# Optimization experiments

Measured on AMD Instinct MI355X. Metric: run time of the kernel, lower is better.

The kernel has to match this reference:

```python
import jax, jax.numpy as jnp
import numpy as np

T, B, H = 2048, 8, 16
KF, VF, KS, VS = 32, 64, 128, 64


def _l2norm(x, eps=1e-6):
    return x / jnp.sqrt(jnp.sum(x * x, axis=-1, keepdims=True) + eps)


def setup_inputs() -> dict:
    key = jax.random.key(0)
    ks = jax.random.split(key, 12)
    # k/q are L2-normalized externally (per E88/E90 kernel contract)
    k_fast = _l2norm(jax.random.normal(ks[0], (T, B, H, KF), jnp.float32))
    q_fast = _l2norm(jax.random.normal(ks[1], (T, B, H, KF), jnp.float32))
    v_fast = jax.random.normal(ks[2], (T, B, H, VF), jnp.float32)
    k_slow = _l2norm(jax.random.normal(ks[3], (T, B, H, KS), jnp.float32))
    q_slow = _l2norm(jax.random.normal(ks[4], (T, B, H, KS), jnp.float32))
    v_slow = jax.random.normal(ks[5], (T, B, H, VS), jnp.float32)
    # decay factors in (0.85, 1.0): typical Mamba2-style per-head scalar decay
    decay_fast = 0.85 + 0.15 * jax.random.uniform(ks[6], (T, B, H), jnp.float32)
    decay_slow = 0.85 + 0.15 * jax.random.uniform(ks[7], (T, B, H), jnp.float32)
    slow_gate = jax.random.uniform(ks[8], (T, B, H), jnp.float32)
    mix_fast = jax.random.uniform(ks[9], (T, B, H), jnp.float32)
    mix_slow = jax.random.uniform(ks[10], (T, B, H), jnp.float32)
    S_fast0 = jnp.zeros((B, H, KF, VF), jnp.float32)
    S_slow0 = jnp.zeros((B, H, KS, VS), jnp.float32)
    return dict(k_fast=k_fast, v_fast=v_fast, q_fast=q_fast, decay_fast=decay_fast,
                k_slow=k_slow, v_slow=v_slow, q_slow=q_slow, decay_slow=decay_slow,
                slow_gate=slow_gate, mix_fast=mix_fast, mix_slow=mix_slow,
                S_fast0=S_fast0, S_slow0=S_slow0, n_heads=H)


def _e90_scan(k_fast, v_fast, q_fast, decay_fast,
              k_slow, v_slow, q_slow, decay_slow,
              slow_gate, mix_fast, mix_slow, S_fast0, S_slow0):
    def step(carry, x):
        S_f, S_s = carry  # [B,H,KF,VF], [B,H,KS,VS]
        kf, vf, qf, df, ksl, vsl, qsl, dsl, g, mf, ms = x
        # fast state: updated every timestep (decay + rank-1 outer product)
        S_f = df[..., None, None] * S_f + kf[..., :, None] * vf[..., None, :]
        # slow state: gated soft update
        S_s_new = dsl[..., None, None] * S_s + ksl[..., :, None] * vsl[..., None, :]
        g_ = g[..., None, None]
        S_s = g_ * S_s_new + (1.0 - g_) * S_s
        out_f = jnp.einsum('bhk,bhkv->bhv', qf, S_f)
        out_s = jnp.einsum('bhk,bhkv->bhv', qsl, S_s)
        out = mf[..., None] * out_f + ms[..., None] * out_s
        return (S_f, S_s), out

    xs = (k_fast, v_fast, q_fast, decay_fast,
          k_slow, v_slow, q_slow, decay_slow,
          slow_gate, mix_fast, mix_slow)
    (S_f_final, S_s_final), output = jax.lax.scan(step, (S_fast0, S_slow0), xs)
    return S_f_final, S_s_final, output  # output: [T,B,H,VF]


def reference(k_fast, v_fast, q_fast, decay_fast, k_slow, v_slow, q_slow,
              decay_slow, slow_gate, mix_fast, mix_slow, S_fast0, S_slow0, n_heads):
    return _e90_scan(k_fast, v_fast, q_fast, decay_fast,
                     k_slow, v_slow, q_slow, decay_slow,
                     slow_gate, mix_fast, mix_slow, S_fast0, S_slow0)
```

## Files before the change

kernel.cpp:

```cpp
#include <hip/hip_runtime.h>

#define T_STEPS 2048
#define BH      128
#define KS_     128
#define VS_     64
#define KF_     32
#define VF_     64
#define LCH     32
#define NCG     32
#define NC      (T_STEPS / LCH)
#define HALF_T  1024
#define NTHR    512
#define NTHRA   256
#define WSLOT   5120
#define SCLS_OFF 1310720
#define SCLF_OFF 1835008
#define RUN_OFF  2359296
#define WS_NEEDED_BYTES ((size_t)(RUN_OFF + 512) * 4)
#define SOFF    (BH*KF_*VF_)
#define YOFF    (BH*KF_*VF_ + BH*KS_*VS_)

typedef __attribute__((ext_vector_type(8))) short short8;
typedef __attribute__((ext_vector_type(16))) float f32x16;

#define MFMA32(a,b,c) __builtin_amdgcn_mfma_f32_32x32x16_bf16((a),(b),(c),0,0,0)
#define CROW(r,hi) (((r)&3) + 8*((r)>>2) + 4*(hi))

__device__ __forceinline__ unsigned short f2b(float x) {
    union { float f; unsigned u; } v; v.f = x;
    unsigned r = v.u + 0x7FFFu + ((v.u >> 16) & 1u);
    return (unsigned short)(r >> 16);
}
__device__ __forceinline__ unsigned cvtpk(float lo, float hi_) {
    unsigned r;
    asm("v_cvt_pk_bf16_f32 %0, %1, %2" : "=v"(r) : "v"(lo), "v"(hi_));
    return r;
}
__device__ __forceinline__ short8 ld8(const unsigned short* p) {
    return *(const short8*)p;
}

__global__ __launch_bounds__(NTHRA, 2)
void e90_scan(const float* __restrict__ k_fast,  const float* __restrict__ v_fast,
              const float* __restrict__ q_fast,  const float* __restrict__ decay_fast,
              const float* __restrict__ k_slow,  const float* __restrict__ v_slow,
              const float* __restrict__ q_slow,  const float* __restrict__ decay_slow,
              const float* __restrict__ slow_gate, const float* __restrict__ mix_fast,
              const float* __restrict__ mix_slow, const float* __restrict__ S_fast0,
              const float* __restrict__ S_slow0, float* __restrict__ dout,
              float* __restrict__ dws)
{
    __shared__ __align__(16) unsigned short Qs [LCH][136];
    __shared__ __align__(16) unsigned short Ksl[LCH][136];
    __shared__ __align__(16) unsigned short Sbs[LCH][136];
    __shared__ __align__(16) unsigned short Psl[LCH][40];
    __shared__ __align__(16) unsigned short Pfl[LCH][40];
    __shared__ __align__(16) unsigned short Qfl[LCH][40];
    __shared__ __align__(16) unsigned short Kfl[LCH][40];
    __shared__ __align__(16) unsigned short Sbfl[LCH][40];
    __shared__ __align__(16) unsigned short VTs[2][LCH][40];
    __shared__ __align__(16) unsigned short VTf[2][LCH][40];

    const int tid  = threadIdx.x;
    const int bid  = blockIdx.x;
    const int xcd  = bid & 7;
    const int q8   = bid >> 3;
    const int p    = xcd * 16 + (q8 >> 2);
    const int vh   = (q8 >> 1) & 1;
    const int v0   = vh * 32;
    const int th   = q8 & 1;
    const int tgb  = th * HALF_T;
    const int slot = p * 2 + vh;
    const int lane = tid & 63;
    const int wid  = tid >> 6;
    const int l31  = lane & 31;
    const int hi   = lane >> 5;
    const int s_   = tid >> 3;
    const int sub  = tid & 7;
    const int k0_  = sub * 16;
    const int j0_  = sub * 4;

    float* out_y = dout + YOFF;

    f32x16 St0, St1, oacc;
#pragma unroll
    for (int r = 0; r < 16; ++r) { St0[r] = 0.0f; St1[r] = 0.0f; oacc[r] = 0.0f; }
    if (th == 0) {
        if (wid < 2) {
#pragma unroll
            for (int r = 0; r < 16; ++r) {
                St0[r] = S_slow0[((size_t)p*KS_ + 32*(2*wid)   + CROW(r,hi))*VS_ + v0 + l31];
                St1[r] = S_slow0[((size_t)p*KS_ + 32*(2*wid+1) + CROW(r,hi))*VS_ + v0 + l31];
            }
        } else if (wid == 2) {
#pragma unroll
            for (int r = 0; r < 16; ++r)
                St0[r] = S_fast0[((size_t)p*KF_ + CROW(r,hi))*VF_ + v0 + l31];
        }
    }
    if (wid < 2) {
#pragma unroll
        for (int r = 0; r < 16; ++r) {
            Sbs[l31][32*(2*wid)   + CROW(r,hi)] = f2b(St0[r]);
            Sbs[l31][32*(2*wid+1) + CROW(r,hi)] = f2b(St1[r]);
        }
    } else if (wid == 2) {
#pragma unroll
        for (int r = 0; r < 16; ++r) Sbfl[l31][CROW(r,hi)] = f2b(St0[r]);
    }

    float4 pK0,pK1,pK2,pK3, pQ0,pQ1,pQ2,pQ3, pVs,pVf,pKf,pQf;
    float pL0 = 0.f, pL1 = 0.f, pL2 = 0.f;

#define LOADCHUNK(CIDX) do {                                                    \
    int tc_ = (CIDX); if (tc_ > NCG-1) tc_ = NCG-1;                             \
    const int tb_ = tgb + tc_ * LCH;                                            \
    const float* bk_ = k_slow + ((size_t)(tb_+s_)*BH + p)*KS_ + k0_;            \
    pK0 = *(const float4*)bk_;      pK1 = *(const float4*)(bk_+4);              \
    pK2 = *(const float4*)(bk_+8);  pK3 = *(const float4*)(bk_+12);             \
    const float* bq_ = q_slow + ((size_t)(tb_+s_)*BH + p)*KS_ + k0_;            \
    pQ0 = *(const float4*)bq_;      pQ1 = *(const float4*)(bq_+4);              \
    pQ2 = *(const float4*)(bq_+8);  pQ3 = *(const float4*)(bq_+12);             \
    pVs = *(const float4*)(v_slow + ((size_t)(tb_+s_)*BH + p)*VS_ + v0 + j0_);  \
    pVf = *(const float4*)(v_fast + ((size_t)(tb_+s_)*BH + p)*VF_ + v0 + j0_);  \
    pKf = *(const float4*)(k_fast + ((size_t)(tb_+s_)*BH + p)*KF_ + j0_);       \
    pQf = *(const float4*)(q_fast + ((size_t)(tb_+s_)*BH + p)*KF_ + j0_);       \
    const size_t so_ = (size_t)(tb_ + l31)*BH + p;                              \
    pL0 = (hi ? decay_fast : decay_slow)[so_];                                  \
    pL1 = (hi ? mix_fast   : slow_gate )[so_];                                  \
    pL2 = hi ? 0.0f : mix_slow[so_];                                            \
    } while (0)

    LOADCHUNK(0);

    float bls = 1.f, blf = 1.f, ib = 1.f, ibf = 1.f, qsc = 0.f, qfc = 0.f, g_s = 0.f;
    float runAcc = 1.0f;

    for (int c = 0; c < NCG; ++c) {
        const int cb = c & 1;
        if (c > 0) {
            if (wid < 2) {
#pragma unroll
                for (int r = 0; r < 16; ++r) {
                    Sbs[l31][32*(2*wid)   + CROW(r,hi)] = f2b(St0[r]);
                    Sbs[l31][32*(2*wid+1) + CROW(r,hi)] = f2b(St1[r]);
                }
            } else if (wid == 2) {
#pragma unroll
                for (int r = 0; r < 16; ++r) Sbfl[l31][CROW(r,hi)] = f2b(St0[r]);
            } else {
                const int pb = cb ^ 1;
                f32x16 o2;
#pragma unroll
                for (int r = 0; r < 16; ++r) o2[r] = 0.0f;
                const unsigned short* ar = &Psl[l31][0];
                const unsigned short* br = &VTs[pb][l31][0];
                oacc = MFMA32(ld8(ar + 8*hi),      ld8(br + 8*hi),      oacc);
                oacc = MFMA32(ld8(ar + 16 + 8*hi), ld8(br + 16 + 8*hi), oacc);
                const unsigned short* af = &Pfl[l31][0];
                const unsigned short* bf = &VTf[pb][l31][0];
                o2 = MFMA32(ld8(af + 8*hi),      ld8(bf + 8*hi),      o2);
                o2 = MFMA32(ld8(af + 16 + 8*hi), ld8(bf + 16 + 8*hi), o2);
#pragma unroll
                for (int r = 0; r < 16; ++r) {
                    int tr = CROW(r,hi);
                    out_y[((size_t)(tgb + (c-1)*LCH + tr)*BH + p)*VF_ + v0 + l31] = oacc[r] + o2[r];
                }
            }
        }
        {
            float a = hi ? pL0 : __builtin_fmaf(pL1, pL0, 1.0f - pL1);
            float b = a;
#pragma unroll
            for (int d = 1; d < 32; d <<= 1) {
                float y = __shfl_up(b, d, 32);
                if (l31 >= d) b *= y;
            }
            if (th == 1 && wid == 0) {
                float sc = (hi ? pL1 : pL2) * b * runAcc;
                float* wsp = dws + (hi ? SCLF_OFF : SCLS_OFF) + (size_t)slot*HALF_T + c*LCH + l31;
                *wsp = sc;
            }
            float bs_s = __shfl(b, s_);
            float bf_s = __shfl(b, 32 + s_);
            bls = __shfl(b, 31);
            blf = __shfl(b, 63);
            g_s = __shfl(pL1, s_);
            float mf_s = __shfl(pL1, 32 + s_);
            float ms_s = __shfl(pL2, s_);
            ib  = 1.0f / bs_s;
            ibf = 1.0f / bf_s;
            qsc = ms_s * bs_s;
            qfc = mf_s * bf_s;
            runAcc *= (hi ? blf : bls);
        }
        {
            uint4 kw0, kw1, qw0, qw1;
            kw0.x = cvtpk(pK0.x*ib, pK0.y*ib);  kw0.y = cvtpk(pK0.z*ib, pK0.w*ib);
            kw0.z = cvtpk(pK1.x*ib, pK1.y*ib);  kw0.w = cvtpk(pK1.z*ib, pK1.w*ib);
            kw1.x = cvtpk(pK2.x*ib, pK2.y*ib);  kw1.y = cvtpk(pK2.z*ib, pK2.w*ib);
            kw1.z = cvtpk(pK3.x*ib, pK3.y*ib);  kw1.w = cvtpk(pK3.z*ib, pK3.w*ib);
            qw0.x = cvtpk(pQ0.x*qsc, pQ0.y*qsc); qw0.y = cvtpk(pQ0.z*qsc, pQ0.w*qsc);
            qw0.z = cvtpk(pQ1.x*qsc, pQ1.y*qsc); qw0.w = cvtpk(pQ1.z*qsc, pQ1.w*qsc);
            qw1.x = cvtpk(pQ2.x*qsc, pQ2.y*qsc); qw1.y = cvtpk(pQ2.z*qsc, pQ2.w*qsc);
            qw1.z = cvtpk(pQ3.x*qsc, pQ3.y*qsc); qw1.w = cvtpk(pQ3.z*qsc, pQ3.w*qsc);
            *(uint4*)&Ksl[s_][k0_]   = kw0;
            *(uint4*)&Ksl[s_][k0_+8] = kw1;
            *(uint4*)&Qs [s_][k0_]   = qw0;
            *(uint4*)&Qs [s_][k0_+8] = qw1;

            VTs[cb][j0_+0][s_] = f2b(g_s*pVs.x);
            VTs[cb][j0_+1][s_] = f2b(g_s*pVs.y);
            VTs[cb][j0_+2][s_] = f2b(g_s*pVs.z);
            VTs[cb][j0_+3][s_] = f2b(g_s*pVs.w);
            VTf[cb][j0_+0][s_] = f2b(pVf.x);
            VTf[cb][j0_+1][s_] = f2b(pVf.y);
            VTf[cb][j0_+2][s_] = f2b(pVf.z);
            VTf[cb][j0_+3][s_] = f2b(pVf.w);
            uint2 kf2; kf2.x = cvtpk(pKf.x*ibf, pKf.y*ibf); kf2.y = cvtpk(pKf.z*ibf, pKf.w*ibf);
            *(uint2*)&Kfl[s_][j0_] = kf2;
            uint2 qf2; qf2.x = cvtpk(pQf.x*qfc, pQf.y*qfc); qf2.y = cvtpk(pQf.z*qfc, pQf.w*qfc);
            *(uint2*)&Qfl[s_][j0_] = qf2;
        }
        __syncthreads();

        LOADCHUNK(c + 1);

        if (wid < 2) {
            const unsigned short* bv = &VTs[cb][l31][0];
            short8 b1 = ld8(bv + 8*hi);
            short8 b2 = ld8(bv + 16 + 8*hi);
            {
                const int T = 2*wid;
                short8 a1, a2;
#pragma unroll
                for (int e = 0; e < 8; ++e) {
                    a1[e] = (short)Ksl[8*hi + e][32*T + l31];
                    a2[e] = (short)Ksl[16 + 8*hi + e][32*T + l31];
                }
                St0 = MFMA32(a1, b1, St0);
                St0 = MFMA32(a2, b2, St0);
#pragma unroll
                for (int r = 0; r < 16; ++r) St0[r] *= bls;
            }
            {
                const int T = 2*wid + 1;
                short8 a1, a2;
#pragma unroll
                for (int e = 0; e < 8; ++e) {
                    a1[e] = (short)Ksl[8*hi + e][32*T + l31];
                    a2[e] = (short)Ksl[16 + 8*hi + e][32*T + l31];
                }
                St1 = MFMA32(a1, b1, St1);
                St1 = MFMA32(a2, b2, St1);
#pragma unroll
                for (int r = 0; r < 16; ++r) St1[r] *= bls;
            }
        } else if (wid == 2) {
            {
                short8 a1, a2;
#pragma unroll
                for (int e = 0; e < 8; ++e) {
                    a1[e] = (short)Kfl[8*hi + e][l31];
                    a2[e] = (short)Kfl[16 + 8*hi + e][l31];
                }
                const unsigned short* bv = &VTf[cb][l31][0];
                St0 = MFMA32(a1, ld8(bv + 8*hi),      St0);
                St0 = MFMA32(a2, ld8(bv + 16 + 8*hi), St0);
#pragma unroll
                for (int r = 0; r < 16; ++r) St0[r] *= blf;
            }
            {
                f32x16 p1;
#pragma unroll
                for (int r = 0; r < 16; ++r) p1[r] = 0.0f;
                const unsigned short* ar = &Qfl[l31][0];
                const unsigned short* br = &Kfl[l31][0];
                p1 = MFMA32(ld8(ar + 8*hi),      ld8(br + 8*hi),      p1);
                p1 = MFMA32(ld8(ar + 16 + 8*hi), ld8(br + 16 + 8*hi), p1);
#pragma unroll
                for (int r = 0; r < 16; ++r) {
                    int tr = CROW(r,hi);
                    Pfl[tr][l31] = f2b(tr >= l31 ? p1[r] : 0.0f);
                }
            }
            {
                f32x16 p1, p2;
#pragma unroll
                for (int r = 0; r < 16; ++r) { p1[r] = 0.0f; p2[r] = 0.0f; }
                const unsigned short* ar = &Qs [l31][0];
                const unsigned short* br = &Ksl[l31][0];
                const int kb = 8*hi;
#pragma unroll
                for (int st = 0; st < 8; st += 2) {
                    p1 = MFMA32(ld8(ar + kb + 16*st),     ld8(br + kb + 16*st),     p1);
                    p2 = MFMA32(ld8(ar + kb + 16*(st+1)), ld8(br + kb + 16*(st+1)), p2);
                }
#pragma unroll
                for (int r = 0; r < 16; ++r) {
                    int tr = CROW(r,hi);
                    Psl[tr][l31] = f2b(tr >= l31 ? p1[r] + p2[r] : 0.0f);
                }
            }
        } else {
            f32x16 o1, o2;
#pragma unroll
            for (int r = 0; r < 16; ++r) { o1[r] = 0.0f; o2[r] = 0.0f; }
            const unsigned short* ar = &Qs [l31][0];
            const unsigned short* br = &Sbs[l31][0];
            const int kb = 8*hi;
#pragma unroll
            for (int st = 0; st < 8; st += 2) {
                o1 = MFMA32(ld8(ar + kb + 16*st),     ld8(br + kb + 16*st),     o1);
                o2 = MFMA32(ld8(ar + kb + 16*(st+1)), ld8(br + kb + 16*(st+1)), o2);
            }
            const unsigned short* af = &Qfl [l31][0];
            const unsigned short* bf = &Sbfl[l31][0];
            o1 = MFMA32(ld8(af + 8*hi),      ld8(bf + 8*hi),      o1);
            o2 = MFMA32(ld8(af + 16 + 8*hi), ld8(bf + 16 + 8*hi), o2);
#pragma unroll
            for (int r = 0; r < 16; ++r) oacc[r] = o1[r] + o2[r];
        }
        __syncthreads();
    }

    if (wid == 3) {
        const int pb = (NCG - 1) & 1;
        f32x16 o2;
#pragma unroll
        for (int r = 0; r < 16; ++r) o2[r] = 0.0f;
        const unsigned short* ar = &Psl[l31][0];
        const unsigned short* br = &VTs[pb][l31][0];
        oacc = MFMA32(ld8(ar + 8*hi),      ld8(br + 8*hi),      oacc);
        oacc = MFMA32(ld8(ar + 16 + 8*hi), ld8(br + 16 + 8*hi), oacc);
        const unsigned short* af = &Pfl[l31][0];
        const unsigned short* bf = &VTf[pb][l31][0];
        o2 = MFMA32(ld8(af + 8*hi),      ld8(bf + 8*hi),      o2);
        o2 = MFMA32(ld8(af + 16 + 8*hi), ld8(bf + 16 + 8*hi), o2);
#pragma unroll
        for (int r = 0; r < 16; ++r) {
            int tr = CROW(r,hi);
            out_y[((size_t)(tgb + (NCG-1)*LCH + tr)*BH + p)*VF_ + v0 + l31] = oacc[r] + o2[r];
        }
    }

    if (th == 0) {
        if (wid < 2) {
#pragma unroll
            for (int r = 0; r < 16; ++r) {
                int cr = CROW(r,hi);
                dout[SOFF + ((size_t)p*KS_ + 32*(2*wid)   + cr)*VS_ + v0 + l31] = St0[r];
                dout[SOFF + ((size_t)p*KS_ + 32*(2*wid+1) + cr)*VS_ + v0 + l31] = St1[r];
            }
        } else if (wid == 2) {
#pragma unroll
            for (int r = 0; r < 16; ++r)
                dout[((size_t)p*KF_ + CROW(r,hi))*VF_ + v0 + l31] = St0[r];
        }
    } else {
        if (wid < 2) {
#pragma unroll
            for (int r = 0; r < 16; ++r) {
                int cr = CROW(r,hi);
                dws[(size_t)slot*WSLOT + (32*(2*wid)   + cr)*32 + l31] = St0[r];
                dws[(size_t)slot*WSLOT + (32*(2*wid+1) + cr)*32 + l31] = St1[r];
            }
        } else if (wid == 2) {
#pragma unroll
            for (int r = 0; r < 16; ++r)
                dws[(size_t)slot*WSLOT + (128 + CROW(r,hi))*32 + l31] = St0[r];
        }
        if (wid == 0 && lane == 0)  dws[RUN_OFF + slot*2 + 0] = runAcc;
        if (wid == 0 && lane == 32) dws[RUN_OFF + slot*2 + 1] = runAcc;
    }
#undef LOADCHUNK
}

__global__ __launch_bounds__(NTHR, 2)
void e90_fix(const float* __restrict__ q_fast, const float* __restrict__ q_slow,
             const float* __restrict__ dws, float* __restrict__ dout)
{
    __shared__ __align__(16) unsigned short SbS[32][136];
    __shared__ __align__(16) unsigned short SbF[32][40];

    const int tid  = threadIdx.x;
    const int bid  = blockIdx.x;
    const int xcd  = bid & 7;
    const int jj   = bid >> 3;
    const int p    = xcd * 16 + (jj >> 1);
    const int vh   = jj & 1;
    const int v0   = vh * 32;
    const int slot = p * 2 + vh;
    const int lane = tid & 63;
    const int w8   = tid >> 6;
    const int l31  = lane & 31;
    const int hi   = lane >> 5;

    float* out_y = dout + YOFF;

    for (int i = tid; i < 128 * 32; i += NTHR) {
        int k = i >> 5, v = i & 31;
        SbS[v][k] = f2b(dout[SOFF + ((size_t)p*KS_ + k)*VS_ + v0 + v]);
    }
    for (int i = tid; i < 32 * 32; i += NTHR) {
        int k = i >> 5, v = i & 31;
        SbF[v][k] = f2b(dout[((size_t)p*KF_ + k)*VF_ + v0 + v]);
    }
    __syncthreads();

    {
        const float runS = dws[RUN_OFF + slot*2 + 0];
        const float runF = dws[RUN_OFF + slot*2 + 1];
        for (int i = tid; i < WSLOT; i += NTHR) {
            int k = i >> 5, v = i & 31;
            float st = dws[(size_t)slot*WSLOT + i];
            if (k < 128) {
                size_t o = SOFF + ((size_t)p*KS_ + k)*VS_ + v0 + v;
                dout[o] = runS * dout[o] + st;
            } else {
                size_t o = ((size_t)p*KF_ + (k - 128))*VF_ + v0 + v;
                dout[o] = runF * dout[o] + st;
            }
        }
    }

#pragma unroll 1
    for (int j = 0; j < 4; ++j) {
        const int cc = w8 * 4 + j;
        const int t0 = HALF_T + cc * LCH;
        const float sS = dws[SCLS_OFF + (size_t)slot*HALF_T + cc*LCH + l31];
        const float sF = dws[SCLF_OFF + (size_t)slot*HALF_T + cc*LCH + l31];
        const size_t so = (size_t)(t0 + l31) * BH + p;
        f32x16 c1, c2;
#pragma unroll
        for (int r = 0; r < 16; ++r) { c1[r] = 0.0f; c2[r] = 0.0f; }
#pragma unroll
        for (int st = 0; st < 8; ++st) {
            const float* qp = q_slow + so*KS_ + 16*st + 8*hi;
            float4 x = *(const float4*)qp;
            float4 y = *(const float4*)(qp + 4);
            union { unsigned u[4]; short8 s; } fr;
            fr.u[0] = cvtpk(x.x*sS, x.y*sS);
            fr.u[1] = cvtpk(x.z*sS, x.w*sS);
            fr.u[2] = cvtpk(y.x*sS, y.y*sS);
            fr.u[3] = cvtpk(y.z*sS, y.w*sS);
            if (st & 1) c2 = MFMA32(fr.s, ld8(&SbS[l31][16*st + 8*hi]), c2);
            else        c1 = MFMA32(fr.s, ld8(&SbS[l31][16*st + 8*hi]), c1);
        }
#pragma unroll
        for (int st = 0; st < 2; ++st) {
            const float* qp = q_fast + so*KF_ + 16*st + 8*hi;
            float4 x = *(const float4*)qp;
            float4 y = *(const float4*)(qp + 4);
            union { unsigned u[4]; short8 s; } fr;
            fr.u[0] = cvtpk(x.x*sF, x.y*sF);
            fr.u[1] = cvtpk(x.z*sF, x.w*sF);
            fr.u[2] = cvtpk(y.x*sF, y.y*sF);
            fr.u[3] = cvtpk(y.z*sF, y.w*sF);
            if (st & 1) c2 = MFMA32(fr.s, ld8(&SbF[l31][16*st + 8*hi]), c2);
            else        c1 = MFMA32(fr.s, ld8(&SbF[l31][16*st + 8*hi]), c1);
        }
#pragma unroll
        for (int r = 0; r < 16; ++r) {
            int tr = CROW(r,hi);
            size_t o = ((size_t)(t0 + tr)*BH + p)*VF_ + v0 + l31;
            out_y[o] += c1[r] + c2[r];
        }
    }
}

__global__ __launch_bounds__(NTHR, 2)
void e90_mono(const float* __restrict__ k_fast,  const float* __restrict__ v_fast,
              const float* __restrict__ q_fast,  const float* __restrict__ decay_fast,
              const float* __restrict__ k_slow,  const float* __restrict__ v_slow,
              const float* __restrict__ q_slow,  const float* __restrict__ decay_slow,
              const float* __restrict__ slow_gate, const float* __restrict__ mix_fast,
              const float* __restrict__ mix_slow, const float* __restrict__ S_fast0,
              const float* __restrict__ S_slow0, float* __restrict__ dout)
{
    __shared__ __align__(16) unsigned short Qs  [2][LCH][136];
    __shared__ __align__(16) unsigned short Ksl [2][LCH][136];
    __shared__ __align__(16) unsigned short Sbs [2][LCH][136];
    __shared__ __align__(16) unsigned short Psl [2][LCH][40];
    __shared__ __align__(16) unsigned short Pfl [2][LCH][40];
    __shared__ __align__(16) unsigned short Qfl [2][LCH][40];
    __shared__ __align__(16) unsigned short Kfl [2][LCH][40];
    __shared__ __align__(16) unsigned short Sbfl[2][LCH][40];
    __shared__ __align__(16) unsigned short VTs [3][LCH][40];
    __shared__ __align__(16) unsigned short VTf [3][LCH][40];

    const int tid  = threadIdx.x;
    const int bid  = blockIdx.x;
    const int xcd  = bid & 7;
    const int jj   = bid >> 3;
    const int p    = xcd * 16 + (jj >> 1);
    const int v0   = (jj & 1) * 32;
    const int lane = tid & 63;
    const int wid  = tid >> 6;
    const int l31  = lane & 31;
    const int hi   = lane >> 5;
    const int s_   = tid >> 4;
    const int j0_  = (tid & 15) * 2;
    const int k0_  = (tid & 15) * 8;

    float* out_y = dout + YOFF;

    f32x16 Sst, oacc;
#pragma unroll
    for (int r = 0; r < 16; ++r) { Sst[r] = 0.0f; oacc[r] = 0.0f; }
    if (wid < 4) {
#pragma unroll
        for (int r = 0; r < 16; ++r)
            Sst[r] = S_slow0[((size_t)p*KS_ + 32*wid + CROW(r,hi))*VS_ + v0 + l31];
#pragma unroll
        for (int r = 0; r < 16; ++r) Sbs[0][l31][32*wid + CROW(r,hi)] = f2b(Sst[r]);
    } else if (wid == 4) {
#pragma unroll
        for (int r = 0; r < 16; ++r)
            Sst[r] = S_fast0[((size_t)p*KF_ + CROW(r,hi))*VF_ + v0 + l31];
#pragma unroll
        for (int r = 0; r < 16; ++r) Sbfl[0][l31][CROW(r,hi)] = f2b(Sst[r]);
    }

    float4 pKs0, pKs1, pQs0, pQs1;
    float2 pVs, pVf, pKf, pQf;
    float pL0 = 0.f, pL1 = 0.f, pL2 = 0.f;
    float bls = 1.f, blf = 1.f, ib = 1.f, ibf = 1.f, qsc = 0.f, qfc = 0.f, g_s = 0.f;

#define LOADVEC(CIDX) do {                                                     \
    int tc_ = (CIDX); if (tc_ > NC-1) tc_ = NC-1;                              \
    const int tb_ = tc_ * LCH;                                                 \
    const float* bk_ = k_slow + ((size_t)(tb_+s_)*BH + p)*KS_ + k0_;           \
    pKs0 = *(const float4*)bk_;  pKs1 = *(const float4*)(bk_+4);               \
    const float* bq_ = q_slow + ((size_t)(tb_+s_)*BH + p)*KS_ + k0_;           \
    pQs0 = *(const float4*)bq_;  pQs1 = *(const float4*)(bq_+4);               \
    pVs = *(const float2*)(v_slow + ((size_t)(tb_+s_)*BH + p)*VS_ + v0 + j0_); \
    pVf = *(const float2*)(v_fast + ((size_t)(tb_+s_)*BH + p)*VF_ + v0 + j0_); \
    pKf = *(const float2*)(k_fast + ((size_t)(tb_+s_)*BH + p)*KF_ + j0_);      \
    pQf = *(const float2*)(q_fast + ((size_t)(tb_+s_)*BH + p)*KF_ + j0_);      \
    } while (0)

#define LOADSCL(CIDX) do {                                                     \
    int tc_ = (CIDX); if (tc_ > NC-1) tc_ = NC-1;                              \
    const size_t so_ = (size_t)(tc_*LCH + l31)*BH + p;                         \
    pL0 = (hi ? decay_fast : decay_slow)[so_];                                 \
    pL1 = (hi ? mix_fast   : slow_gate )[so_];                                 \
    pL2 = hi ? 0.0f : mix_slow[so_];                                           \
    } while (0)

#define SCAN() do {                                                            \
    float a_ = hi ? pL0 : __builtin_fmaf(pL1, pL0, 1.0f - pL1);                \
    float b_ = a_;                                                             \
    _Pragma("unroll")                                                          \
    for (int d = 1; d < 32; d <<= 1) {                                         \
        float y_ = __shfl_up(b_, d, 32);                                       \
        if (l31 >= d) b_ *= y_;                                                \
    }                                                                          \
    float bs_s = __shfl(b_, s_);                                               \
    float bf_s = __shfl(b_, 32 + s_);                                          \
    bls = __shfl(b_, 31);                                                      \
    blf = __shfl(b_, 63);                                                      \
    g_s = __shfl(pL1, s_);                                                     \
    float mf_s = __shfl(pL1, 32 + s_);                                         \
    float ms_s = __shfl(pL2, s_);                                              \
    ib  = 1.0f / bs_s;                                                         \
    ibf = 1.0f / bf_s;                                                         \
    qsc = ms_s * bs_s;                                                         \
    qfc = mf_s * bf_s;                                                         \
    } while (0)

#define STAGE(J2, J3) do {                                                     \
    uint4 kw, qw;                                                              \
    kw.x = cvtpk(pKs0.x*ib, pKs0.y*ib);  kw.y = cvtpk(pKs0.z*ib, pKs0.w*ib);   \
    kw.z = cvtpk(pKs1.x*ib, pKs1.y*ib);  kw.w = cvtpk(pKs1.z*ib, pKs1.w*ib);   \
    qw.x = cvtpk(pQs0.x*qsc, pQs0.y*qsc); qw.y = cvtpk(pQs0.z*qsc, pQs0.w*qsc);\
    qw.z = cvtpk(pQs1.x*qsc, pQs1.y*qsc); qw.w = cvtpk(pQs1.z*qsc, pQs1.w*qsc);\
    *(uint4*)&Ksl[J2][s_][k0_] = kw;                                           \
    *(uint4*)&Qs [J2][s_][k0_] = qw;                                           \
    float vt0 = g_s*pVs.x, vt1 = g_s*pVs.y;                                    \
    VTs[J3][j0_  ][s_] = f2b(vt0);                                             \
    VTs[J3][j0_+1][s_] = f2b(vt1);                                             \
    VTf[J3][j0_  ][s_] = f2b(pVf.x);                                           \
    VTf[J3][j0_+1][s_] = f2b(pVf.y);                                           \
    unsigned kfp = cvtpk(pKf.x*ibf, pKf.y*ibf);                                \
    *(unsigned*)&Kfl[J2][s_][j0_] = kfp;                                       \
    unsigned qfp = cvtpk(pQf.x*qfc, pQf.y*qfc);                                \
    *(unsigned*)&Qfl[J2][s_][j0_] = qfp;                                       \
    } while (0)

#define YSTORE(CP) do {                                                        \
    const int p2_ = (CP) & 1, p3_ = (CP) % 3;                                  \
    f32x16 o2;                                                                 \
    _Pragma("unroll")                                                          \
    for (int r = 0; r < 16; ++r) o2[r] = 0.0f;                                 \
    const unsigned short* ar = &Psl[p2_][l31][0];                              \
    const unsigned short* br = &VTs[p3_][l31][0];                              \
    oacc = MFMA32(ld8(ar + 8*hi),      ld8(br + 8*hi),      oacc);             \
    oacc = MFMA32(ld8(ar + 16 + 8*hi), ld8(br + 16 + 8*hi), oacc);             \
    const unsigned short* af = &Pfl[p2_][l31][0];                              \
    const unsigned short* bf = &VTf[p3_][l31][0];                              \
    o2 = MFMA32(ld8(af + 8*hi),      ld8(bf + 8*hi),      o2);                 \
    o2 = MFMA32(ld8(af + 16 + 8*hi), ld8(bf + 16 + 8*hi), o2);                 \
    _Pragma("unroll")                                                          \
    for (int r = 0; r < 16; ++r) {                                             \
        int tr = CROW(r,hi);                                                   \
        out_y[((size_t)((CP)*LCH + tr)*BH + p)*VF_ + v0 + l31] = oacc[r] + o2[r]; \
    }                                                                          \
    } while (0)

    LOADVEC(0);
    LOADSCL(0);
    SCAN();
    LOADSCL(1);
    STAGE(0, 0);
    __syncthreads();

    for (int c = 0; c < NC; ++c) {
        const int i2 = c & 1;
        const int i3 = c % 3;
        LOADVEC(c + 1);

        if (wid < 4) {
            short8 a1, a2;
#pragma unroll
            for (int e = 0; e < 8; ++e) {
                a1[e] = (short)Ksl[i2][8*hi + e][32*wid + l31];
                a2[e] = (short)Ksl[i2][16 + 8*hi + e][32*wid + l31];
            }
            const unsigned short* br = &VTs[i3][l31][0];
            Sst = MFMA32(a1, ld8(br + 8*hi),      Sst);
            Sst = MFMA32(a2, ld8(br + 16 + 8*hi), Sst);
#pragma unroll
            for (int r = 0; r < 16; ++r) Sst[r] *= bls;
        } else if (wid == 4) {
            short8 a1, a2;
#pragma unroll
            for (int e = 0; e < 8; ++e) {
                a1[e] = (short)Kfl[i2][8*hi + e][l31];
                a2[e] = (short)Kfl[i2][16 + 8*hi + e][l31];
            }
            const unsigned short* br = &VTf[i3][l31][0];
            Sst = MFMA32(a1, ld8(br + 8*hi),      Sst);
            Sst = MFMA32(a2, ld8(br + 16 + 8*hi), Sst);
#pragma unroll
            for (int r = 0; r < 16; ++r) Sst[r] *= blf;
        } else if (wid == 5) {
            f32x16 p1, p2;
#pragma unroll
            for (int r = 0; r < 16; ++r) { p1[r] = 0.0f; p2[r] = 0.0f; }
            const unsigned short* ar = &Qs [i2][l31][0];
            const unsigned short* br = &Ksl[i2][l31][0];
            const int kb = 8*hi;
#pragma unroll
            for (int st = 0; st < 8; st += 2) {
                p1 = MFMA32(ld8(ar + kb + 16*st),     ld8(br + kb + 16*st),     p1);
                p2 = MFMA32(ld8(ar + kb + 16*(st+1)), ld8(br + kb + 16*(st+1)), p2);
            }
#pragma unroll
            for (int r = 0; r < 16; ++r) {
                int tr = CROW(r,hi);
                Psl[i2][tr][l31] = f2b(tr >= l31 ? p1[r] + p2[r] : 0.0f);
            }
        } else if (wid == 6) {
            f32x16 p1;
#pragma unroll
            for (int r = 0; r < 16; ++r) p1[r] = 0.0f;
            const unsigned short* ar = &Qfl[i2][l31][0];
            const unsigned short* br = &Kfl[i2][l31][0];
            p1 = MFMA32(ld8(ar + 8*hi),      ld8(br + 8*hi),      p1);
            p1 = MFMA32(ld8(ar + 16 + 8*hi), ld8(br + 16 + 8*hi), p1);
#pragma unroll
            for (int r = 0; r < 16; ++r) {
                int tr = CROW(r,hi);
                Pfl[i2][tr][l31] = f2b(tr >= l31 ? p1[r] : 0.0f);
            }
        } else {
            if (c > 0) YSTORE(c - 1);
            f32x16 o1, o2;
#pragma unroll
            for (int r = 0; r < 16; ++r) { o1[r] = 0.0f; o2[r] = 0.0f; }
            const unsigned short* ar = &Qs [i2][l31][0];
            const unsigned short* br = &Sbs[i2][l31][0];
            const int kb = 8*hi;
#pragma unroll
            for (int st = 0; st < 8; st += 2) {
                o1 = MFMA32(ld8(ar + kb + 16*st),     ld8(br + kb + 16*st),     o1);
                o2 = MFMA32(ld8(ar + kb + 16*(st+1)), ld8(br + kb + 16*(st+1)), o2);
            }
            const unsigned short* af = &Qfl [i2][l31][0];
            const unsigned short* bf = &Sbfl[i2][l31][0];
            o1 = MFMA32(ld8(af + 8*hi),      ld8(bf + 8*hi),      o1);
            o2 = MFMA32(ld8(af + 16 + 8*hi), ld8(bf + 16 + 8*hi), o2);
#pragma unroll
            for (int r = 0; r < 16; ++r) oacc[r] = o1[r] + o2[r];
        }

        SCAN();
        LOADSCL(c + 2);

        if (c < NC - 1) {
            const int j2 = (c + 1) & 1;
            const int j3 = (c + 1) % 3;
            if (wid < 4) {
#pragma unroll
                for (int r = 0; r < 16; ++r) Sbs[j2][l31][32*wid + CROW(r,hi)] = f2b(Sst[r]);
            } else if (wid == 4) {
#pragma unroll
                for (int r = 0; r < 16; ++r) Sbfl[j2][l31][CROW(r,hi)] = f2b(Sst[r]);
            }
            STAGE(j2, j3);
        }
        __syncthreads();
    }

    if (wid == 7) {
        YSTORE(NC - 1);
    }
    if (wid < 4) {
#pragma unroll
        for (int r = 0; r < 16; ++r)
            dout[SOFF + ((size_t)p*KS_ + 32*wid + CROW(r,hi))*VS_ + v0 + l31] = Sst[r];
    } else if (wid == 4) {
#pragma unroll
        for (int r = 0; r < 16; ++r)
            dout[((size_t)p*KF_ + CROW(r,hi))*VF_ + v0 + l31] = Sst[r];
    }
#undef LOADVEC
#undef LOADSCL
#undef SCAN
#undef STAGE
#undef YSTORE
}

extern "C" void kernel_launch(void* const* d_in, const int* in_sizes, int n_in,
                              void* d_out, int out_size, void* d_ws, size_t ws_size,
                              hipStream_t stream)
{
    const float* k_fast     = (const float*)d_in[0];
    const float* v_fast     = (const float*)d_in[1];
    const float* q_fast     = (const float*)d_in[2];
    const float* decay_fast = (const float*)d_in[3];
    const float* k_slow     = (const float*)d_in[4];
    const float* v_slow     = (const float*)d_in[5];
    const float* q_slow     = (const float*)d_in[6];
    const float* decay_slow = (const float*)d_in[7];
    const float* slow_gate  = (const float*)d_in[8];
    const float* mix_fast   = (const float*)d_in[9];
    const float* mix_slow   = (const float*)d_in[10];
    const float* S_fast0    = (const float*)d_in[11];
    const float* S_slow0    = (const float*)d_in[12];
    float* dout = (float*)d_out;
    float* dws  = (float*)d_ws;

    if (ws_size >= WS_NEEDED_BYTES) {
        e90_scan<<<dim3(512), dim3(NTHRA), 0, stream>>>(
            k_fast, v_fast, q_fast, decay_fast,
            k_slow, v_slow, q_slow, decay_slow,
            slow_gate, mix_fast, mix_slow, S_fast0, S_slow0, dout, dws);
        e90_fix<<<dim3(256), dim3(NTHR), 0, stream>>>(q_fast, q_slow, dws, dout);
    } else {
        e90_mono<<<dim3(256), dim3(NTHR), 0, stream>>>(
            k_fast, v_fast, q_fast, decay_fast,
            k_slow, v_slow, q_slow, decay_slow,
            slow_gate, mix_fast, mix_slow, S_fast0, S_slow0, dout);
    }
}
```

Baseline: 206.8 us.

## Merge both time-half scan blocks into one 512-thread workgroup

The scan kernel now launches 256 workgroups of 512 threads instead of 512 of 256. Each workgroup processes both time halves for one (head, v-half) pair, with each 256-thread group using its own copy of the shared-memory buffers. The likely aim is to cut workgroup count and scheduling overhead and co-locate the two halves that read the same head's inputs. In exchange, __syncthreads now couples both halves, shared memory per block doubles, and the 512-thread launch bound may limit registers per thread.

After: 212.2 us. +2.6%, slower.

```diff
diff --git a/kernel.cpp b/kernel.cpp
--- a/kernel.cpp
+++ b/kernel.cpp
@@ -11,7 +11,6 @@
 #define NC      (T_STEPS / LCH)
 #define HALF_T  1024
 #define NTHR    512
-#define NTHRA   256
 #define WSLOT   5120
 #define SCLS_OFF 1310720
 #define SCLF_OFF 1835008
@@ -40,7 +39,7 @@
     return *(const short8*)p;
 }
 
-__global__ __launch_bounds__(NTHRA, 2)
+__global__ __launch_bounds__(NTHR, 2)
 void e90_scan(const float* __restrict__ k_fast,  const float* __restrict__ v_fast,
               const float* __restrict__ q_fast,  const float* __restrict__ decay_fast,
               const float* __restrict__ k_slow,  const float* __restrict__ v_slow,
@@ -50,35 +49,36 @@
               const float* __restrict__ S_slow0, float* __restrict__ dout,
               float* __restrict__ dws)
 {
-    __shared__ __align__(16) unsigned short Qs [LCH][136];
-    __shared__ __align__(16) unsigned short Ksl[LCH][136];
-    __shared__ __align__(16) unsigned short Sbs[LCH][136];
-    __shared__ __align__(16) unsigned short Psl[LCH][40];
-    __shared__ __align__(16) unsigned short Pfl[LCH][40];
-    __shared__ __align__(16) unsigned short Qfl[LCH][40];
-    __shared__ __align__(16) unsigned short Kfl[LCH][40];
-    __shared__ __align__(16) unsigned short Sbfl[LCH][40];
-    __shared__ __align__(16) unsigned short VTs[2][LCH][40];
-    __shared__ __align__(16) unsigned short VTf[2][LCH][40];
+    __shared__ __align__(16) unsigned short Qs  [2][LCH][136];
+    __shared__ __align__(16) unsigned short Ksl [2][LCH][136];
+    __shared__ __align__(16) unsigned short Sbs [2][LCH][136];
+    __shared__ __align__(16) unsigned short Psl [2][LCH][40];
+    __shared__ __align__(16) unsigned short Pfl [2][LCH][40];
+    __shared__ __align__(16) unsigned short Qfl [2][LCH][40];
+    __shared__ __align__(16) unsigned short Kfl [2][LCH][40];
+    __shared__ __align__(16) unsigned short Sbfl[2][LCH][40];
+    __shared__ __align__(16) unsigned short VTs [2][2][LCH][40];
+    __shared__ __align__(16) unsigned short VTf [2][2][LCH][40];
 
     const int tid  = threadIdx.x;
+    const int th   = tid >> 8;
+    const int gtid = tid & 255;
+    const int wid4 = (tid >> 6) & 3;
+    const int lane = tid & 63;
+    const int l31  = lane & 31;
+    const int hi   = lane >> 5;
+    const int s_   = gtid >> 3;
+    const int sub  = gtid & 7;
+    const int k0_  = sub * 16;
+    const int j0_  = sub * 4;
     const int bid  = blockIdx.x;
     const int xcd  = bid & 7;
-    const int q8   = bid >> 3;
-    const int p    = xcd * 16 + (q8 >> 2);
-    const int vh   = (q8 >> 1) & 1;
+    const int jj   = bid >> 3;
+    const int p    = xcd * 16 + (jj >> 1);
+    const int vh   = jj & 1;
     const int v0   = vh * 32;
-    const int th   = q8 & 1;
+    const int slot = p * 2 + vh;
     const int tgb  = th * HALF_T;
-    const int slot = p * 2 + vh;
-    const int lane = tid & 63;
-    const int wid  = tid >> 6;
-    const int l31  = lane & 31;
-    const int hi   = lane >> 5;
-    const int s_   = tid >> 3;
-    const int sub  = tid & 7;
-    const int k0_  = sub * 16;
-    const int j0_  = sub * 4;
 
     float* out_y = dout + YOFF;
 
@@ -86,27 +86,27 @@
 #pragma unroll
     for (int r = 0; r < 16; ++r) { St0[r] = 0.0f; St1[r] = 0.0f; oacc[r] = 0.0f; }
     if (th == 0) {
-        if (wid < 2) {
+        if (wid4 < 2) {
 #pragma unroll
             for (int r = 0; r < 16; ++r) {
-                St0[r] = S_slow0[((size_t)p*KS_ + 32*(2*wid)   + CROW(r,hi))*VS_ + v0 + l31];
-                St1[r] = S_slow0[((size_t)p*KS_ + 32*(2*wid+1) + CROW(r,hi))*VS_ + v0 + l31];
-            }
-        } else if (wid == 2) {
+                St0[r] = S_slow0[((size_t)p*KS_ + 32*(2*wid4)   + CROW(r,hi))*VS_ + v0 + l31];
+                St1[r] = S_slow0[((size_t)p*KS_ + 32*(2*wid4+1) + CROW(r,hi))*VS_ + v0 + l31];
+            }
+        } else if (wid4 == 2) {
 #pragma unroll
             for (int r = 0; r < 16; ++r)
                 St0[r] = S_fast0[((size_t)p*KF_ + CROW(r,hi))*VF_ + v0 + l31];
         }
     }
-    if (wid < 2) {
+    if (wid4 < 2) {
 #pragma unroll
         for (int r = 0; r < 16; ++r) {
-            Sbs[l31][32*(2*wid)   + CROW(r,hi)] = f2b(St0[r]);
-            Sbs[l31][32*(2*wid+1) + CROW(r,hi)] = f2b(St1[r]);
-        }
-    } else if (wid == 2) {
-#pragma unroll
-        for (int r = 0; r < 16; ++r) Sbfl[l31][CROW(r,hi)] = f2b(St0[r]);
+            Sbs[th][l31][32*(2*wid4)   + CROW(r,hi)] = f2b(St0[r]);
+            Sbs[th][l31][32*(2*wid4+1) + CROW(r,hi)] = f2b(St1[r]);
+        }
+    } else if (wid4 == 2) {
+#pragma unroll
+        for (int r = 0; r < 16; ++r) Sbfl[th][l31][CROW(r,hi)] = f2b(St0[r]);
     }
 
     float4 pK0,pK1,pK2,pK3, pQ0,pQ1,pQ2,pQ3, pVs,pVf,pKf,pQf;
@@ -139,26 +139,26 @@
     for (int c = 0; c < NCG; ++c) {
         const int cb = c & 1;
         if (c > 0) {
-            if (wid < 2) {
+            if (wid4 < 2) {
 #pragma unroll
                 for (int r = 0; r < 16; ++r) {
-                    Sbs[l31][32*(2*wid)   + CROW(r,hi)] = f2b(St0[r]);
-                    Sbs[l31][32*(2*wid+1) + CROW(r,hi)] = f2b(St1[r]);
+                    Sbs[th][l31][32*(2*wid4)   + CROW(r,hi)] = f2b(St0[r]);
+                    Sbs[th][l31][32*(2*wid4+1) + CROW(r,hi)] = f2b(St1[r]);
                 }
-            } else if (wid == 2) {
-#pragma unroll
-                for (int r = 0; r < 16; ++r) Sbfl[l31][CROW(r,hi)] = f2b(St0[r]);
+            } else if (wid4 == 2) {
+#pragma unroll
+                for (int r = 0; r < 16; ++r) Sbfl[th][l31][CROW(r,hi)] = f2b(St0[r]);
             } else {
                 const int pb = cb ^ 1;
                 f32x16 o2;
 #pragma unroll
                 for (int r = 0; r < 16; ++r) o2[r] = 0.0f;
-                const unsigned short* ar = &Psl[l31][0];
-                const unsigned short* br = &VTs[pb][l31][0];
+                const unsigned short* ar = &Psl[th][l31][0];
+                const unsigned short* br = &VTs[th][pb][l31][0];
                 oacc = MFMA32(ld8(ar + 8*hi),      ld8(br + 8*hi),      oacc);
                 oacc = MFMA32(ld8(ar + 16 + 8*hi), ld8(br + 16 + 8*hi), oacc);
-                const unsigned short* af = &Pfl[l31][0];
-                const unsigned short* bf = &VTf[pb][l31][0];
+                const unsigned short* af = &Pfl[th][l31][0];
+                const unsigned short* bf = &VTf[th][pb][l31][0];
                 o2 = MFMA32(ld8(af + 8*hi),      ld8(bf + 8*hi),      o2);
                 o2 = MFMA32(ld8(af + 16 + 8*hi), ld8(bf + 16 + 8*hi), o2);
 #pragma unroll
@@ -176,7 +176,7 @@
                 float y = __shfl_up(b, d, 32);
                 if (l31 >= d) b *= y;
             }
-            if (th == 1 && wid == 0) {
+            if (th == 1 && wid4 == 0) {
                 float sc = (hi ? pL1 : pL2) * b * runAcc;
                 float* wsp = dws + (hi ? SCLF_OFF : SCLS_OFF) + (size_t)slot*HALF_T + c*LCH + l31;
                 *wsp = sc;
@@ -204,39 +204,39 @@
             qw0.z = cvtpk(pQ1.x*qsc, pQ1.y*qsc); qw0.w = cvtpk(pQ1.z*qsc, pQ1.w*qsc);
             qw1.x = cvtpk(pQ2.x*qsc, pQ2.y*qsc); qw1.y = cvtpk(pQ2.z*qsc, pQ2.w*qsc);
             qw1.z = cvtpk(pQ3.x*qsc, pQ3.y*qsc); qw1.w = cvtpk(pQ3.z*qsc, pQ3.w*qsc);
-            *(uint4*)&Ksl[s_][k0_]   = kw0;
-            *(uint4*)&Ksl[s_][k0_+8] = kw1;
-            *(uint4*)&Qs [s_][k0_]   = qw0;
-            *(uint4*)&Qs [s_][k0_+8] = qw1;
-
-            VTs[cb][j0_+0][s_] = f2b(g_s*pVs.x);
-            VTs[cb][j0_+1][s_] = f2b(g_s*pVs.y);
-            VTs[cb][j0_+2][s_] = f2b(g_s*pVs.z);
-            VTs[cb][j0_+3][s_] = f2b(g_s*pVs.w);
-            VTf[cb][j0_+0][s_] = f2b(pVf.x);
-            VTf[cb][j0_+1][s_] = f2b(pVf.y);
-            VTf[cb][j0_+2][s_] = f2b(pVf.z);
-            VTf[cb][j0_+3][s_] = f2b(pVf.w);
+            *(uint4*)&Ksl[th][s_][k0_]   = kw0;
+            *(uint4*)&Ksl[th][s_][k0_+8] = kw1;
+            *(uint4*)&Qs [th][s_][k0_]   = qw0;
+            *(uint4*)&Qs [th][s_][k0_+8] = qw1;
+
+            VTs[th][cb][j0_+0][s_] = f2b(g_s*pVs.x);
+            VTs[th][cb][j0_+1][s_] = f2b(g_s*pVs.y);
+            VTs[th][cb][j0_+2][s_] = f2b(g_s*pVs.z);
+            VTs[th][cb][j0_+3][s_] = f2b(g_s*pVs.w);
+            VTf[th][cb][j0_+0][s_] = f2b(pVf.x);
+            VTf[th][cb][j0_+1][s_] = f2b(pVf.y);
+            VTf[th][cb][j0_+2][s_] = f2b(pVf.z);
+            VTf[th][cb][j0_+3][s_] = f2b(pVf.w);
             uint2 kf2; kf2.x = cvtpk(pKf.x*ibf, pKf.y*ibf); kf2.y = cvtpk(pKf.z*ibf, pKf.w*ibf);
-            *(uint2*)&Kfl[s_][j0_] = kf2;
+            *(uint2*)&Kfl[th][s_][j0_] = kf2;
             uint2 qf2; qf2.x = cvtpk(pQf.x*qfc, pQf.y*qfc); qf2.y = cvtpk(pQf.z*qfc, pQf.w*qfc);
-            *(uint2*)&Qfl[s_][j0_] = qf2;
+            *(uint2*)&Qfl[th][s_][j0_] = qf2;
         }
         __syncthreads();
 
         LOADCHUNK(c + 1);
 
-        if (wid < 2) {
-            const unsigned short* bv = &VTs[cb][l31][0];
+        if (wid4 < 2) {
+            const unsigned short* bv = &VTs[th][cb][l31][0];
             short8 b1 = ld8(bv + 8*hi);
             short8 b2 = ld8(bv + 16 + 8*hi);
             {
-                const int T = 2*wid;
+                const int T = 2*wid4;
                 short8 a1, a2;
 #pragma unroll
                 for (int e = 0; e < 8; ++e) {
-                    a1[e] = (short)Ksl[8*hi + e][32*T + l31];
-                    a2[e] = (short)Ksl[16 + 8*hi + e][32*T + l31];
+                    a1[e] = (short)Ksl[th][8*hi + e][32*T + l31];
+                    a2[e] = (short)Ksl[th][16 + 8*hi + e][32*T + l31];
                 }
                 St0 = MFMA32(a1, b1, St0);
                 St0 = MFMA32(a2, b2, St0);
@@ -244,27 +244,27 @@
                 for (int r = 0; r < 16; ++r) St0[r] *= bls;
             }
             {
-                const int T = 2*wid + 1;
+                const int T = 2*wid4 + 1;
                 short8 a1, a2;
 #pragma unroll
                 for (int e = 0; e < 8; ++e) {
-                    a1[e] = (short)Ksl[8*hi + e][32*T + l31];
-                    a2[e] = (short)Ksl[16 + 8*hi + e][32*T + l31];
+                    a1[e] = (short)Ksl[th][8*hi + e][32*T + l31];
+                    a2[e] = (short)Ksl[th][16 + 8*hi + e][32*T + l31];
                 }
                 St1 = MFMA32(a1, b1, St1);
                 St1 = MFMA32(a2, b2, St1);
 #pragma unroll
                 for (int r = 0; r < 16; ++r) St1[r] *= bls;
             }
-        } else if (wid == 2) {
+        } else if (wid4 == 2) {
             {
                 short8 a1, a2;
 #pragma unroll
                 for (int e = 0; e < 8; ++e) {
-                    a1[e] = (short)Kfl[8*hi + e][l31];
-                    a2[e] = (short)Kfl[16 + 8*hi + e][l31];
+                    a1[e] = (short)Kfl[th][8*hi + e][l31];
+                    a2[e] = (short)Kfl[th][16 + 8*hi + e][l31];
                 }
-                const unsigned short* bv = &VTf[cb][l31][0];
+                const unsigned short* bv = &VTf[th][cb][l31][0];
                 St0 = MFMA32(a1, ld8(bv + 8*hi),      St0);
                 St0 = MFMA32(a2, ld8(bv + 16 + 8*hi), St0);
 #pragma unroll
@@ -274,22 +274,22 @@
                 f32x16 p1;
 #pragma unroll
                 for (int r = 0; r < 16; ++r) p1[r] = 0.0f;
-                const unsigned short* ar = &Qfl[l31][0];
-                const unsigned short* br = &Kfl[l31][0];
+                const unsigned short* ar = &Qfl[th][l31][0];
+                const unsigned short* br = &Kfl[th][l31][0];
                 p1 = MFMA32(ld8(ar + 8*hi),      ld8(br + 8*hi),      p1);
                 p1 = MFMA32(ld8(ar + 16 + 8*hi), ld8(br + 16 + 8*hi), p1);
 #pragma unroll
                 for (int r = 0; r < 16; ++r) {
                     int tr = CROW(r,hi);
-                    Pfl[tr][l31] = f2b(tr >= l31 ? p1[r] : 0.0f);
+                    Pfl[th][tr][l31] = f2b(tr >= l31 ? p1[r] : 0.0f);
                 }
             }
             {
                 f32x16 p1, p2;
 #pragma unroll
                 for (int r = 0; r < 16; ++r) { p1[r] = 0.0f; p2[r] = 0.0f; }
-                const unsigned short* ar = &Qs [l31][0];
-                const unsigned short* br = &Ksl[l31][0];
+                const unsigned short* ar = &Qs [th][l31][0];
+                const unsigned short* br = &Ksl[th][l31][0];
                 const int kb = 8*hi;
 #pragma unroll
                 for (int st = 0; st < 8; st += 2) {
@@ -299,23 +299,23 @@
 #pragma unroll
                 for (int r = 0; r < 16; ++r) {
                     int tr = CROW(r,hi);
-                    Psl[tr][l31] = f2b(tr >= l31 ? p1[r] + p2[r] : 0.0f);
+                    Psl[th][tr][l31] = f2b(tr >= l31 ? p1[r] + p2[r] : 0.0f);
                 }
             }
         } else {
             f32x16 o1, o2;
 #pragma unroll
             for (int r = 0; r < 16; ++r) { o1[r] = 0.0f; o2[r] = 0.0f; }
-            const unsigned short* ar = &Qs [l31][0];
-            const unsigned short* br = &Sbs[l31][0];
+            const unsigned short* ar = &Qs [th][l31][0];
+            const unsigned short* br = &Sbs[th][l31][0];
             const int kb = 8*hi;
 #pragma unroll
             for (int st = 0; st < 8; st += 2) {
                 o1 = MFMA32(ld8(ar + kb + 16*st),     ld8(br + kb + 16*st),     o1);
                 o2 = MFMA32(ld8(ar + kb + 16*(st+1)), ld8(br + kb + 16*(st+1)), o2);
             }
-            const unsigned short* af = &Qfl [l31][0];
-            const unsigned short* bf = &Sbfl[l31][0];
+            const unsigned short* af = &Qfl [th][l31][0];
+            const unsigned short* bf = &Sbfl[th][l31][0];
             o1 = MFMA32(ld8(af + 8*hi),      ld8(bf + 8*hi),      o1);
             o2 = MFMA32(ld8(af + 16 + 8*hi), ld8(bf + 16 + 8*hi), o2);
 #pragma unroll
@@ -324,17 +324,17 @@
         __syncthreads();
     }
 
-    if (wid == 3) {
+    if (wid4 == 3) {
         const int pb = (NCG - 1) & 1;
         f32x16 o2;
 #pragma unroll
         for (int r = 0; r < 16; ++r) o2[r] = 0.0f;
-        const unsigned short* ar = &Psl[l31][0];
-        const unsigned short* br = &VTs[pb][l31][0];
+        const unsigned short* ar = &Psl[th][l31][0];
+        const unsigned short* br = &VTs[th][pb][l31][0];
         oacc = MFMA32(ld8(ar + 8*hi),      ld8(br + 8*hi),      oacc);
         oacc = MFMA32(ld8(ar + 16 + 8*hi), ld8(br + 16 + 8*hi), oacc);
-        const unsigned short* af = &Pfl[l31][0];
-        const unsigned short* bf = &VTf[pb][l31][0];
+        const unsigned short* af = &Pfl[th][l31][0];
+        const unsigned short* bf = &VTf[th][pb][l31][0];
         o2 = MFMA32(ld8(af + 8*hi),      ld8(bf + 8*hi),      o2);
         o2 = MFMA32(ld8(af + 16 + 8*hi), ld8(bf + 16 + 8*hi), o2);
 #pragma unroll
@@ -345,33 +345,33 @@
     }
 
     if (th == 0) {
-        if (wid < 2) {
+        if (wid4 < 2) {
 #pragma unroll
             for (int r = 0; r < 16; ++r) {
                 int cr = CROW(r,hi);
-                dout[SOFF + ((size_t)p*KS_ + 32*(2*wid)   + cr)*VS_ + v0 + l31] = St0[r];
-                dout[SOFF + ((size_t)p*KS_ + 32*(2*wid+1) + cr)*VS_ + v0 + l31] = St1[r];
-            }
-        } else if (wid == 2) {
+                dout[SOFF + ((size_t)p*KS_ + 32*(2*wid4)   + cr)*VS_ + v0 + l31] = St0[r];
+                dout[SOFF + ((size_t)p*KS_ + 32*(2*wid4+1) + cr)*VS_ + v0 + l31] = St1[r];
+            }
+        } else if (wid4 == 2) {
 #pragma unroll
             for (int r = 0; r < 16; ++r)
                 dout[((size_t)p*KF_ + CROW(r,hi))*VF_ + v0 + l31] = St0[r];
         }
     } else {
-        if (wid < 2) {
+        if (wid4 < 2) {
 #pragma unroll
             for (int r = 0; r < 16; ++r) {
                 int cr = CROW(r,hi);
-                dws[(size_t)slot*WSLOT + (32*(2*wid)   + cr)*32 + l31] = St0[r];
-                dws[(size_t)slot*WSLOT + (32*(2*wid+1) + cr)*32 + l31] = St1[r];
-            }
-        } else if (wid == 2) {
+                dws[(size_t)slot*WSLOT + (32*(2*wid4)   + cr)*32 + l31] = St0[r];
+                dws[(size_t)slot*WSLOT + (32*(2*wid4+1) + cr)*32 + l31] = St1[r];
+            }
+        } else if (wid4 == 2) {
 #pragma unroll
             for (int r = 0; r < 16; ++r)
                 dws[(size_t)slot*WSLOT + (128 + CROW(r,hi))*32 + l31] = St0[r];
         }
-        if (wid == 0 && lane == 0)  dws[RUN_OFF + slot*2 + 0] = runAcc;
-        if (wid == 0 && lane == 32) dws[RUN_OFF + slot*2 + 1] = runAcc;
+        if (wid4 == 0 && lane == 0)  dws[RUN_OFF + slot*2 + 0] = runAcc;
+        if (wid4 == 0 && lane == 32) dws[RUN_OFF + slot*2 + 1] = runAcc;
     }
 #undef LOADCHUNK
 }
@@ -753,7 +753,7 @@
     float* dws  = (float*)d_ws;
 
     if (ws_size >= WS_NEEDED_BYTES) {
-        e90_scan<<<dim3(512), dim3(NTHRA), 0, stream>>>(
+        e90_scan<<<dim3(256), dim3(NTHR), 0, stream>>>(
             k_fast, v_fast, q_fast, decay_fast,
             k_slow, v_slow, q_slow, decay_slow,
             slow_gate, mix_fast, mix_slow, S_fast0, S_slow0, dout, dws);
```
